# Kernel optimization log

Measured on AMD Instinct MI355X. Metric: run time of the kernel, lower is better.

Reference implementation:

```python
import jax, jax.numpy as jnp
import numpy as np

T, B, H = 2048, 32, 1024


def setup_inputs() -> dict:
    key = jax.random.key(0)
    k1, k2, k3 = jax.random.split(key, 3)
    t_input = jax.random.normal(k1, (T, B, H), dtype=jnp.float32)
    h0 = jax.random.normal(k2, (B, H), dtype=jnp.float32)
    # weight_hh ~ U(0, 1) per reset_parameters default
    weight_hh = jax.random.uniform(k3, (H,), dtype=jnp.float32)
    return {"t_input": t_input, "h0": h0, "weight_hh": weight_hh}


def reference(t_input, h0, weight_hh):
    # h_t = relu(x_t + whh * h_{t-1}); per-channel recurrent scan over time.
    def step(h, x):
        h_new = jax.nn.relu(x + weight_hh * h)  # (B, H)
        return h_new, h_new

    _, out = jax.lax.scan(step, h0, t_input)  # out: (T, B, H)
    return out
```

## Files before the change

### kernel.cpp

```cpp
#include <hip/hip_runtime.h>


#define T_STEPS 2048
#define B_DIM   32
#define H_DIM   1024
#define BH      (B_DIM * H_DIM)
#define BH2     (BH / 2)
#define PF      32

typedef float f2 __attribute__((ext_vector_type(2)));

__global__ __launch_bounds__(64, 1)
void indrnn_kernel(const f2* __restrict__ x,
                   const f2* __restrict__ h0,
                   const f2* __restrict__ w,
                   f2* __restrict__ out)
{
    const int c2 = blockIdx.x * 64 + threadIdx.x;
    const f2 wv = w[c2 & (H_DIM / 2 - 1)];
    f2 h = h0[c2];

    const f2* xp = x + c2;
    f2* op = out + c2;

    f2 buf[PF];
#pragma unroll
    for (int i = 0; i < PF; ++i)
        buf[i] = __builtin_nontemporal_load(&xp[(size_t)i * BH2]);

    int t0 = 0;
    for (; t0 + PF < T_STEPS; t0 += PF) {
        f2 nxt[PF];
        const int tn = t0 + PF;
#pragma unroll
        for (int i = 0; i < PF; ++i)
            nxt[i] = __builtin_nontemporal_load(&xp[(size_t)(tn + i) * BH2]);

#pragma unroll
        for (int i = 0; i < PF; ++i) {
            h.x = fmaxf(fmaf(wv.x, h.x, buf[i].x), 0.0f);
            h.y = fmaxf(fmaf(wv.y, h.y, buf[i].y), 0.0f);
            __builtin_nontemporal_store(h, &op[(size_t)(t0 + i) * BH2]);
        }

#pragma unroll
        for (int i = 0; i < PF; ++i)
            buf[i] = nxt[i];
    }

#pragma unroll
    for (int i = 0; i < PF; ++i) {
        h.x = fmaxf(fmaf(wv.x, h.x, buf[i].x), 0.0f);
        h.y = fmaxf(fmaf(wv.y, h.y, buf[i].y), 0.0f);
        __builtin_nontemporal_store(h, &op[(size_t)(t0 + i) * BH2]);
    }
}

extern "C" void kernel_launch(void* const* d_in, const int* in_sizes, int n_in,
                              void* d_out, int out_size, void* d_ws, size_t ws_size,
                              hipStream_t stream) {
    const f2* x  = (const f2*)d_in[0];
    const f2* h0 = (const f2*)d_in[1];
    const f2* w  = (const f2*)d_in[2];
    f2* out = (f2*)d_out;

    indrnn_kernel<<<BH2 / 64, 64, 0, stream>>>(x, h0, w, out);
}
```

Measured before the change: 422.8 us.

## Split the recurrence into time segments with a three-phase parallel scan

Replaces the single sequential scan with three kernels. Phase A summarizes each 64-step segment per channel as an affine-plus-max map (M, C, W). Phase B chains those summaries sequentially over the 32 segments to get each segment's starting state. Phase C replays each segment in parallel and writes the outputs. This exposes far more parallelism than the original 256-wavefront launch, which could not saturate memory bandwidth, at the cost of reading the input twice and using a 16 MB workspace. The segment composition is only exact when the weights are non-negative, which holds for the uniform(0,1) initialization. If the workspace is too small, the code falls back to a simpler direct kernel.

```diff
diff --git a/kernel.cpp b/kernel.cpp
--- a/kernel.cpp
+++ b/kernel.cpp
@@ -6,53 +6,140 @@
 #define H_DIM   1024
 #define BH      (B_DIM * H_DIM)
 #define BH2     (BH / 2)
-#define PF      32
+#define SEG     32
+#define SEG_L   (T_STEPS / SEG)
+#define PF      8
 
 typedef float f2 __attribute__((ext_vector_type(2)));
 
+__global__ __launch_bounds__(256)
+void indrnn_phaseA(const f2* __restrict__ x, const f2* __restrict__ w,
+                   f2* __restrict__ Mv, f2* __restrict__ Cv, f2* __restrict__ Wv)
+{
+    const int b  = blockIdx.x;
+    const int s  = b >> 6;
+    const int c2 = ((b & 63) << 8) + threadIdx.x;
+    const f2 wv = w[c2 & (H_DIM / 2 - 1)];
+    const f2* xp = x + (size_t)s * SEG_L * BH2 + c2;
+
+    f2 buf[PF], nxt[PF];
+#pragma unroll
+    for (int i = 0; i < PF; ++i) buf[i] = xp[(size_t)i * BH2];
+#pragma unroll
+    for (int i = 0; i < PF; ++i) nxt[i] = xp[(size_t)(PF + i) * BH2];
+
+    f2 m, cc, Wc;
+    m.x = 0.f; m.y = 0.f;
+    cc = buf[0];
+    Wc = wv;
+#pragma unroll
+    for (int i = 1; i < PF; ++i) {
+        m.x  = fmaxf(0.f, fmaf(wv.x, m.x, buf[i].x));
+        m.y  = fmaxf(0.f, fmaf(wv.y, m.y, buf[i].y));
+        cc.x = fmaf(wv.x, cc.x, buf[i].x);
+        cc.y = fmaf(wv.y, cc.y, buf[i].y);
+        Wc.x *= wv.x; Wc.y *= wv.y;
+    }
+#pragma unroll
+    for (int i = 0; i < PF; ++i) buf[i] = nxt[i];
+
+    for (int t0 = PF; t0 + PF < SEG_L; t0 += PF) {
+#pragma unroll
+        for (int i = 0; i < PF; ++i) nxt[i] = xp[(size_t)(t0 + PF + i) * BH2];
+#pragma unroll
+        for (int i = 0; i < PF; ++i) {
+            m.x  = fmaxf(0.f, fmaf(wv.x, m.x, buf[i].x));
+            m.y  = fmaxf(0.f, fmaf(wv.y, m.y, buf[i].y));
+            cc.x = fmaf(wv.x, cc.x, buf[i].x);
+            cc.y = fmaf(wv.y, cc.y, buf[i].y);
+            Wc.x *= wv.x; Wc.y *= wv.y;
+        }
+#pragma unroll
+        for (int i = 0; i < PF; ++i) buf[i] = nxt[i];
+    }
+#pragma unroll
+    for (int i = 0; i < PF; ++i) {
+        m.x  = fmaxf(0.f, fmaf(wv.x, m.x, buf[i].x));
+        m.y  = fmaxf(0.f, fmaf(wv.y, m.y, buf[i].y));
+        cc.x = fmaf(wv.x, cc.x, buf[i].x);
+        cc.y = fmaf(wv.y, cc.y, buf[i].y);
+        Wc.x *= wv.x; Wc.y *= wv.y;
+    }
+
+    const size_t o = (size_t)s * BH2 + c2;
+    Mv[o] = m; Cv[o] = cc; Wv[o] = Wc;
+}
+
+__global__ __launch_bounds__(256)
+void indrnn_phaseB(const f2* __restrict__ h0, const f2* __restrict__ Mv,
+                   const f2* __restrict__ Cv, const f2* __restrict__ Wv,
+                   f2* __restrict__ Hs)
+{
+    const int c2 = blockIdx.x * 256 + threadIdx.x;
+    f2 h = h0[c2];
+    for (int s = 0; s < SEG; ++s) {
+        const size_t o = (size_t)s * BH2 + c2;
+        Hs[o] = h;
+        const f2 M = Mv[o];
+        const f2 C = Cv[o];
+        const f2 W = Wv[o];
+        h.x = fmaxf(M.x, fmaf(W.x, h.x, C.x));
+        h.y = fmaxf(M.y, fmaf(W.y, h.y, C.y));
+    }
+}
+
+__global__ __launch_bounds__(256)
+void indrnn_phaseC(const f2* __restrict__ x, const f2* __restrict__ w,
+                   const f2* __restrict__ Hs, f2* __restrict__ out)
+{
+    const int b  = blockIdx.x;
+    const int s  = b >> 6;
+    const int c2 = ((b & 63) << 8) + threadIdx.x;
+    const f2 wv = w[c2 & (H_DIM / 2 - 1)];
+    const size_t base = (size_t)s * SEG_L * BH2 + c2;
+    const f2* xp = x + base;
+    f2* op = out + base;
+    f2 h = Hs[(size_t)s * BH2 + c2];
+
+    f2 buf[PF], nxt[PF];
+#pragma unroll
+    for (int i = 0; i < PF; ++i) buf[i] = xp[(size_t)i * BH2];
+
+    for (int t0 = 0; t0 + PF < SEG_L; t0 += PF) {
+#pragma unroll
+        for (int i = 0; i < PF; ++i) nxt[i] = xp[(size_t)(t0 + PF + i) * BH2];
+#pragma unroll
+        for (int i = 0; i < PF; ++i) {
+            h.x = fmaxf(0.f, fmaf(wv.x, h.x, buf[i].x));
+            h.y = fmaxf(0.f, fmaf(wv.y, h.y, buf[i].y));
+            __builtin_nontemporal_store(h, &op[(size_t)(t0 + i) * BH2]);
+        }
+#pragma unroll
+        for (int i = 0; i < PF; ++i) buf[i] = nxt[i];
+    }
+    const int t0f = SEG_L - PF;
+#pragma unroll
+    for (int i = 0; i < PF; ++i) {
+        h.x = fmaxf(0.f, fmaf(wv.x, h.x, buf[i].x));
+        h.y = fmaxf(0.f, fmaf(wv.y, h.y, buf[i].y));
+        __builtin_nontemporal_store(h, &op[(size_t)(t0f + i) * BH2]);
+    }
+}
+
 __global__ __launch_bounds__(64, 1)
-void indrnn_kernel(const f2* __restrict__ x,
-                   const f2* __restrict__ h0,
-                   const f2* __restrict__ w,
-                   f2* __restrict__ out)
+void indrnn_direct(const f2* __restrict__ x, const f2* __restrict__ h0,
+                   const f2* __restrict__ w, f2* __restrict__ out)
 {
     const int c2 = blockIdx.x * 64 + threadIdx.x;
     const f2 wv = w[c2 & (H_DIM / 2 - 1)];
     f2 h = h0[c2];
-
     const f2* xp = x + c2;
     f2* op = out + c2;
-
-    f2 buf[PF];
-#pragma unroll
-    for (int i = 0; i < PF; ++i)
-        buf[i] = __builtin_nontemporal_load(&xp[(size_t)i * BH2]);
-
-    int t0 = 0;
-    for (; t0 + PF < T_STEPS; t0 += PF) {
-        f2 nxt[PF];
-        const int tn = t0 + PF;
-#pragma unroll
-        for (int i = 0; i < PF; ++i)
-            nxt[i] = __builtin_nontemporal_load(&xp[(size_t)(tn + i) * BH2]);
-
-#pragma unroll
-        for (int i = 0; i < PF; ++i) {
-            h.x = fmaxf(fmaf(wv.x, h.x, buf[i].x), 0.0f);
-            h.y = fmaxf(fmaf(wv.y, h.y, buf[i].y), 0.0f);
-            __builtin_nontemporal_store(h, &op[(size_t)(t0 + i) * BH2]);
-        }
-
-#pragma unroll
-        for (int i = 0; i < PF; ++i)
-            buf[i] = nxt[i];
-    }
-
-#pragma unroll
-    for (int i = 0; i < PF; ++i) {
-        h.x = fmaxf(fmaf(wv.x, h.x, buf[i].x), 0.0f);
-        h.y = fmaxf(fmaf(wv.y, h.y, buf[i].y), 0.0f);
-        __builtin_nontemporal_store(h, &op[(size_t)(t0 + i) * BH2]);
+    for (int t = 0; t < T_STEPS; ++t) {
+        f2 xv = xp[(size_t)t * BH2];
+        h.x = fmaxf(0.f, fmaf(wv.x, h.x, xv.x));
+        h.y = fmaxf(0.f, fmaf(wv.y, h.y, xv.y));
+        op[(size_t)t * BH2] = h;
     }
 }
 
@@ -64,5 +151,18 @@
     const f2* w  = (const f2*)d_in[2];
     f2* out = (f2*)d_out;
 
-    indrnn_kernel<<<BH2 / 64, 64, 0, stream>>>(x, h0, w, out);
+    const size_t arr = (size_t)SEG * BH2;
+    const size_t need = 4 * arr * sizeof(f2);
+
+    if (ws_size >= need) {
+        f2* Mv = (f2*)d_ws;
+        f2* Cv = Mv + arr;
+        f2* Wv = Cv + arr;
+        f2* Hs = Wv + arr;
+        indrnn_phaseA<<<SEG * 64, 256, 0, stream>>>(x, w, Mv, Cv, Wv);
+        indrnn_phaseB<<<BH2 / 256, 256, 0, stream>>>(h0, Mv, Cv, Wv, Hs);
+        indrnn_phaseC<<<SEG * 64, 256, 0, stream>>>(x, w, Hs, out);
+    } else {
+        indrnn_direct<<<BH2 / 64, 64, 0, stream>>>(x, h0, w, out);
+    }
 }
```

Result: slower. 490.5 us (+16.0%).
